# Kernel tuning notes

Hardware: AMD Instinct MI355X
Metric: run time of the kernel (lower is better)

Reference implementation:

```python
import jax, jax.numpy as jnp
import numpy as np

D_MODEL = 1024
N_HEADS = 16
D_K = D_MODEL // N_HEADS
D_FF = 4096
B = 2
T = 2048


def _layernorm(x, gamma, beta, eps=1e-5):
    mu = jnp.mean(x, axis=-1, keepdims=True)
    var = jnp.var(x, axis=-1, keepdims=True)
    return (x - mu) * jax.lax.rsqrt(var + eps) * gamma + beta


def _attention(q_in, kv_in, Wq, bq, Wk, bk, Wv, bv, mask):
    # q_in: [B,Tq,D], kv_in: [B,Tk,D]; Wq/Wk/Wv: [H,D,d_k]; b*: [H,d_k]
    Q = jnp.einsum('btd,hdk->bhtk', q_in, Wq) + bq[None, :, None, :]
    K = jnp.einsum('bsd,hdk->bhsk', kv_in, Wk) + bk[None, :, None, :]
    V = jnp.einsum('bsd,hdk->bhsk', kv_in, Wv) + bv[None, :, None, :]
    scores = jnp.einsum('bhtk,bhsk->bhts', Q, K) / jnp.sqrt(jnp.asarray(D_K, Q.dtype))
    if mask is not None:
        scores = jnp.where(mask, scores, jnp.finfo(scores.dtype).min)
    attn = jax.nn.softmax(scores, axis=-1)
    out = jnp.einsum('bhts,bhsk->bhtk', attn, V)  # [B,H,Tq,d_k]
    # concat heads: [B,Tq,H*d_k] == [B,Tq,D]
    return out.transpose(0, 2, 1, 3).reshape(q_in.shape[0], q_in.shape[1], -1)


def setup_inputs() -> dict:
    key = jax.random.key(0)
    ks = jax.random.split(key, 24)
    s = 0.02
    inp = {
        'dec_input': jax.random.normal(ks[0], (B, T, D_MODEL), jnp.float32),
        'enc_output': jax.random.normal(ks[1], (B, T, D_MODEL), jnp.float32),
        # self-attention per-head weights stacked over heads
        'Wq_s': jax.random.normal(ks[2], (N_HEADS, D_MODEL, D_K), jnp.float32) * s,
        'bq_s': jnp.zeros((N_HEADS, D_K), jnp.float32),
        'Wk_s': jax.random.normal(ks[3], (N_HEADS, D_MODEL, D_K), jnp.float32) * s,
        'bk_s': jnp.zeros((N_HEADS, D_K), jnp.float32),
        'Wv_s': jax.random.normal(ks[4], (N_HEADS, D_MODEL, D_K), jnp.float32) * s,
        'bv_s': jnp.zeros((N_HEADS, D_K), jnp.float32),
        'Wo_s': jax.random.normal(ks[5], (D_MODEL, D_MODEL), jnp.float32) * s,
        'bo_s': jnp.zeros((D_MODEL,), jnp.float32),
        # cross-attention per-head weights
        'Wq_c': jax.random.normal(ks[6], (N_HEADS, D_MODEL, D_K), jnp.float32) * s,
        'bq_c': jnp.zeros((N_HEADS, D_K), jnp.float32),
        'Wk_c': jax.random.normal(ks[7], (N_HEADS, D_MODEL, D_K), jnp.float32) * s,
        'bk_c': jnp.zeros((N_HEADS, D_K), jnp.float32),
        'Wv_c': jax.random.normal(ks[8], (N_HEADS, D_MODEL, D_K), jnp.float32) * s,
        'bv_c': jnp.zeros((N_HEADS, D_K), jnp.float32),
        'Wo_c': jax.random.normal(ks[9], (D_MODEL, D_MODEL), jnp.float32) * s,
        'bo_c': jnp.zeros((D_MODEL,), jnp.float32),
        # FFN
        'W1': jax.random.normal(ks[10], (D_MODEL, D_FF), jnp.float32) * s,
        'b1': jnp.zeros((D_FF,), jnp.float32),
        'W2': jax.random.normal(ks[11], (D_FF, D_MODEL), jnp.float32) * s,
        'b2': jnp.zeros((D_MODEL,), jnp.float32),
        # layernorms
        'g1': jnp.ones((D_MODEL,), jnp.float32), 'be1': jnp.zeros((D_MODEL,), jnp.float32),
        'g2': jnp.ones((D_MODEL,), jnp.float32), 'be2': jnp.zeros((D_MODEL,), jnp.float32),
        'g3': jnp.ones((D_MODEL,), jnp.float32), 'be3': jnp.zeros((D_MODEL,), jnp.float32),
    }
    return inp


def reference(dec_input, enc_output,
              Wq_s, bq_s, Wk_s, bk_s, Wv_s, bv_s, Wo_s, bo_s,
              Wq_c, bq_c, Wk_c, bk_c, Wv_c, bv_c, Wo_c, bo_c,
              W1, b1, W2, b2, g1, be1, g2, be2, g3, be3):
    Tq = dec_input.shape[1]
    causal = jnp.tril(jnp.ones((Tq, Tq), bool))[None, None, :, :]  # [1,1,T,T]
    # masked multi-head self-attention (dropout is identity in eval)
    sa = _attention(dec_input, dec_input, Wq_s, bq_s, Wk_s, bk_s, Wv_s, bv_s, causal)
    sa = sa @ Wo_s.T if False else jnp.einsum('btd,ed->bte', sa, Wo_s.T) if False else sa @ Wo_s + bo_s
    x1 = _layernorm(dec_input + sa, g1, be1)
    # cross-attention (no mask)
    ca = _attention(x1, enc_output, Wq_c, bq_c, Wk_c, bk_c, Wv_c, bv_c, None)
    ca = ca @ Wo_c + bo_c
    x2 = _layernorm(x1 + ca, g2, be2)
    # FFN
    ffn = jax.nn.relu(x2 @ W1 + b1) @ W2 + b2
    x3 = _layernorm(x2 + ffn, g3, be3)
    return x3
```

## Files before the change

### kernel.cpp

```cpp
#include <hip/hip_runtime.h>
#include <hip/hip_bf16.h>

typedef __attribute__((ext_vector_type(8))) short short8;
typedef __attribute__((ext_vector_type(4))) short short4v;
typedef __attribute__((ext_vector_type(4))) float floatx4;

#define TDIM 2048
#define BDIM 2
#define MROWS (BDIM * TDIM)

#define ASM_VMCNT0() __asm__ volatile("s_waitcnt vmcnt(0)" ::: "memory")
#define ASM_LGKM0()  __asm__ volatile("s_waitcnt lgkmcnt(0)" ::: "memory")
#define ASM_BARRIER() __asm__ volatile("s_barrier" ::: "memory")

__device__ __forceinline__ floatx4 mfma16(short4v a, short4v b, floatx4 c) {
#if defined(__HIP_DEVICE_COMPILE__)
#if __has_builtin(__builtin_amdgcn_mfma_f32_16x16x16bf16_1k)
    return __builtin_amdgcn_mfma_f32_16x16x16bf16_1k(a, b, c, 0, 0, 0);
#else
    short8 az = {a[0], a[1], a[2], a[3], 0, 0, 0, 0};
    short8 bz = {b[0], b[1], b[2], b[3], 0, 0, 0, 0};
    return __builtin_amdgcn_mfma_f32_16x16x32_bf16(az, bz, c, 0, 0, 0);
#endif
#else
    (void)a; (void)b;
    return c;
#endif
}

__device__ __forceinline__ void gload_lds16(const void* g, void* l) {
    __builtin_amdgcn_global_load_lds((const __attribute__((address_space(1))) void*)g,
                                     (__attribute__((address_space(3))) void*)l, 16, 0, 0);
}

__device__ __forceinline__ short bf16s(float x) {
    __hip_bfloat16 h = __float2bfloat16(x);
    return *(short*)&h;
}

__device__ __forceinline__ float fexp2(float x) {
#if defined(__HIP_DEVICE_COMPILE__)
#if __has_builtin(__builtin_amdgcn_exp2f)
    return __builtin_amdgcn_exp2f(x);
#else
    return exp2f(x);
#endif
#else
    return x;
#endif
}

__global__ __launch_bounds__(256) void cast2_k(const float* __restrict__ a,
                                               const float* __restrict__ b,
                                               __hip_bfloat16* __restrict__ oa,
                                               __hip_bfloat16* __restrict__ ob) {
    const int blk = blockIdx.x;
    const float* in = (blk < 4096) ? a : b;
    __hip_bfloat16* out = (blk < 4096) ? oa : ob;
    const size_t base = (size_t)(blk & 4095) * 1024 + threadIdx.x * 4;
    float4 v = *(const float4*)&in[base];
    out[base + 0] = __float2bfloat16(v.x);
    out[base + 1] = __float2bfloat16(v.y);
    out[base + 2] = __float2bfloat16(v.z);
    out[base + 3] = __float2bfloat16(v.w);
}

__device__ __forceinline__ void t32(float (*tile)[33], const float* __restrict__ in,
                                    __hip_bfloat16* __restrict__ out, int R, int C,
                                    int c0, int r0) {
    const int tx = threadIdx.x & 31, ty = threadIdx.x >> 5;
#pragma unroll
    for (int i = 0; i < 4; ++i)
        tile[ty + 8 * i][tx] = in[(size_t)(r0 + ty + 8 * i) * C + c0 + tx];
    __syncthreads();
#pragma unroll
    for (int i = 0; i < 4; ++i)
        out[(size_t)(c0 + ty + 8 * i) * R + r0 + tx] = __float2bfloat16(tile[tx][ty + 8 * i]);
}

__global__ __launch_bounds__(256) void prep_w_k(
    const float* __restrict__ Wq_s, const float* __restrict__ Wk_s, const float* __restrict__ Wv_s,
    const float* __restrict__ Wq_c, const float* __restrict__ Wk_c, const float* __restrict__ Wv_c,
    const float* __restrict__ Wo_s, const float* __restrict__ Wo_c,
    const float* __restrict__ W1, const float* __restrict__ W2,
    const float* __restrict__ bq_s, const float* __restrict__ bk_s, const float* __restrict__ bv_s,
    const float* __restrict__ bk_c, const float* __restrict__ bv_c,
    __hip_bfloat16* __restrict__ WtQKVs, __hip_bfloat16* __restrict__ WtQc,
    __hip_bfloat16* __restrict__ WtKVc, __hip_bfloat16* __restrict__ WtOs,
    __hip_bfloat16* __restrict__ WtOc, __hip_bfloat16* __restrict__ Wt1,
    __hip_bfloat16* __restrict__ Wt2,
    float* __restrict__ BiasQKVs, float* __restrict__ BiasKVc) {
    __shared__ float tile[32][33];
    const int t = blockIdx.x;
    if (t < 6144) {
        const int seg = t >> 10, tl = t & 1023;
        const float* s;
        __hip_bfloat16* d;
        if (seg == 0) { s = Wq_s; d = WtQKVs; }
        else if (seg == 1) { s = Wk_s; d = WtQKVs + 1048576; }
        else if (seg == 2) { s = Wv_s; d = WtQKVs + 2097152; }
        else if (seg == 3) { s = Wq_c; d = WtQc; }
        else if (seg == 4) { s = Wk_c; d = WtKVc; }
        else { s = Wv_c; d = WtKVc + 1048576; }
        const int slab = tl >> 6, rem = tl & 63;
        t32(tile, s + (size_t)slab * 65536, d + (size_t)slab * 65536, 1024, 64,
            (rem & 1) * 32, (rem >> 1) * 32);
    } else if (t < 8192) {
        const int rem = (t - 6144) & 1023;
        const float* s = (t < 7168) ? Wo_s : Wo_c;
        __hip_bfloat16* d = (t < 7168) ? WtOs : WtOc;
        t32(tile, s, d, 1024, 1024, (rem & 31) * 32, (rem >> 5) * 32);
    } else if (t < 12288) {
        const int rem = t - 8192;
        t32(tile, W1, Wt1, 1024, 4096, (rem & 127) * 32, (rem >> 7) * 32);
    } else if (t < 16384) {
        const int rem = t - 12288;
        t32(tile, W2, Wt2, 4096, 1024, (rem & 31) * 32, (rem >> 5) * 32);
    } else if (t < 16396) {
        const int i = (t - 16384) * 256 + threadIdx.x;
        BiasQKVs[i] = (i < 1024) ? bq_s[i] : (i < 2048 ? bk_s[i - 1024] : bv_s[i - 2048]);
    } else {
        const int i = (t - 16396) * 256 + threadIdx.x;
        BiasKVc[i] = (i < 1024) ? bk_c[i] : bv_c[i - 1024];
    }
}

__device__ __forceinline__ void gemm_core(
    const __hip_bfloat16* __restrict__ A, const __hip_bfloat16* __restrict__ Bt,
    int K, int kBeg, int kLen,
    const float* __restrict__ bias, __hip_bfloat16* __restrict__ C, int ldc,
    float* __restrict__ Pf,
    __hip_bfloat16* __restrict__ Vt, int vt_col0, int relu,
    int m0, int n0, __hip_bfloat16* sm) {
    const int tid = threadIdx.x;
    const int lane = tid & 63, wave = tid >> 6;
    const int quad = lane >> 4, l16 = lane & 15;
    const int wm = (wave >> 1) * 64, wn = (wave & 1) * 64;
    const int lrow = lane >> 3;
    const int gsw = (((lane & 7) ^ lrow)) * 8;
    const int sw7 = l16 & 7;
    const __hip_bfloat16* gA = A + (size_t)(m0 + wave * 32 + lrow) * K + kBeg + gsw;
    const __hip_bfloat16* gB = Bt + (size_t)(n0 + wave * 32 + lrow) * K + kBeg + gsw;
    __hip_bfloat16* lA = sm + wave * 2048;
    __hip_bfloat16* lB = sm + 16384 + wave * 2048;
    floatx4 acc[4][4] = {};
    const int T = kLen >> 6;
#pragma unroll
    for (int i = 0; i < 4; ++i) {
        gload_lds16(gA + (size_t)i * 8 * K, lA + i * 512);
        gload_lds16(gB + (size_t)i * 8 * K, lB + i * 512);
    }
    for (int t = 0; t < T; ++t) {
        ASM_VMCNT0();
        ASM_BARRIER();
        if (t + 1 < T) {
            const int koff = (t + 1) << 6;
            const int b = ((t + 1) & 1) * 8192;
#pragma unroll
            for (int i = 0; i < 4; ++i) {
                gload_lds16(gA + (size_t)i * 8 * K + koff, lA + b + i * 512);
                gload_lds16(gB + (size_t)i * 8 * K + koff, lB + b + i * 512);
            }
        }
        const __hip_bfloat16* cA = sm + (t & 1) * 8192;
        const __hip_bfloat16* cB = sm + 16384 + (t & 1) * 8192;
#pragma unroll
        for (int kc = 0; kc < 2; ++kc) {
            short8 af[4], bfr[4];
#pragma unroll
            for (int i = 0; i < 4; ++i) {
                af[i] = *(const short8*)&cA[(wm + i * 16 + l16) * 64 +
                                            (((kc * 4 + quad) ^ sw7) * 8)];
                bfr[i] = *(const short8*)&cB[(wn + i * 16 + l16) * 64 +
                                             (((kc * 4 + quad) ^ sw7) * 8)];
            }
#pragma unroll
            for (int mi = 0; mi < 4; ++mi)
#pragma unroll
                for (int ni = 0; ni < 4; ++ni)
                    acc[mi][ni] =
                        __builtin_amdgcn_mfma_f32_16x16x32_bf16(af[mi], bfr[ni], acc[mi][ni], 0, 0, 0);
        }
    }
    if (Pf) {
#pragma unroll
        for (int ni = 0; ni < 4; ++ni) {
            const int col = n0 + wn + ni * 16 + l16;
#pragma unroll
            for (int mi = 0; mi < 4; ++mi)
#pragma unroll
                for (int r = 0; r < 4; ++r) {
                    const int row = m0 + wm + mi * 16 + quad * 4 + r;
                    Pf[(size_t)row * ldc + col] = acc[mi][ni][r];
                }
        }
    } else {
        const bool toVt = (n0 >= vt_col0);
#pragma unroll
        for (int ni = 0; ni < 4; ++ni) {
            const int col = n0 + wn + ni * 16 + l16;
            const float bv = bias[col];
#pragma unroll
            for (int mi = 0; mi < 4; ++mi) {
                const int row0 = m0 + wm + mi * 16 + quad * 4;
                if (toVt) {
                    const int b = row0 >> 11, t0 = row0 & (TDIM - 1);
                    short4v pk;
#pragma unroll
                    for (int r = 0; r < 4; ++r) pk[r] = bf16s(acc[mi][ni][r] + bv);
                    *(short4v*)&Vt[((size_t)(b * 1024 + (col - vt_col0)) << 11) + t0] = pk;
                } else {
#pragma unroll
                    for (int r = 0; r < 4; ++r) {
                        float v = acc[mi][ni][r] + bv;
                        if (relu) v = fmaxf(v, 0.f);
                        C[(size_t)(row0 + r) * ldc + col] = __float2bfloat16(v);
                    }
                }
            }
        }
    }
}

__global__ __launch_bounds__(256) void gemm_bf16_k(const __hip_bfloat16* __restrict__ A,
                                                   const __hip_bfloat16* __restrict__ Bt,
                                                   const float* __restrict__ bias,
                                                   __hip_bfloat16* __restrict__ C,
                                                   int N, int K, int relu,
                                                   __hip_bfloat16* __restrict__ Vt, int vt_col0) {
    __shared__ __hip_bfloat16 sm[2 * 128 * 64 * 2];
    gemm_core(A, Bt, K, 0, K, bias, C, N, nullptr, Vt, vt_col0, relu,
              blockIdx.y * 128, blockIdx.x * 128, sm);
}

__global__ __launch_bounds__(256) void gemm_sk2_k(const __hip_bfloat16* __restrict__ A,
                                                  const __hip_bfloat16* __restrict__ Bt,
                                                  float* __restrict__ Pf, int N, int K) {
    __shared__ __hip_bfloat16 sm[2 * 128 * 64 * 2];
    const int z = blockIdx.z;
    gemm_core(A, Bt, K, z * (K >> 1), K >> 1, nullptr, nullptr, N,
              Pf + (size_t)z * MROWS * N, nullptr, 1 << 30, 0,
              blockIdx.y * 128, blockIdx.x * 128, sm);
}

__global__ __launch_bounds__(256) void gemm_pair_k(
    const __hip_bfloat16* __restrict__ A1, const __hip_bfloat16* __restrict__ Bt1,
    const float* __restrict__ bias1, __hip_bfloat16* __restrict__ C1, int N1, int K1,
    const __hip_bfloat16* __restrict__ A2, const __hip_bfloat16* __restrict__ Bt2,
    const float* __restrict__ bias2, __hip_bfloat16* __restrict__ C2, int N2, int K2,
    __hip_bfloat16* __restrict__ Vt2, int vtc2, int nx1) {
    __shared__ __hip_bfloat16 sm[2 * 128 * 64 * 2];
    if ((int)blockIdx.x < nx1)
        gemm_core(A1, Bt1, K1, 0, K1, bias1, C1, N1, nullptr, nullptr, 1 << 30, 0,
                  blockIdx.y * 128, blockIdx.x * 128, sm);
    else
        gemm_core(A2, Bt2, K2, 0, K2, bias2, C2, N2, nullptr, Vt2, vtc2, 0,
                  blockIdx.y * 128, (blockIdx.x - nx1) * 128, sm);
}

__device__ __forceinline__ void flash_one(
    const __hip_bfloat16* __restrict__ Q, int ldq, int qc0,
    const __hip_bfloat16* __restrict__ Kp, int ldk,
    const __hip_bfloat16* __restrict__ Vp,
    __hip_bfloat16* __restrict__ O, int causal, int q0, size_t rowb, int h,
    int tBeg, int tEnd, float* __restrict__ Opart, float* __restrict__ lpart,
    __hip_bfloat16* sK, __hip_bfloat16* sV) {
    const int tid = threadIdx.x, lane = tid & 63, wave = tid >> 6;
    const int quad = lane >> 4, l16 = lane & 15;
    const int lrow = lane >> 3;
    const int gsw = ((lane & 7) ^ lrow) * 8;
    const int sw7 = l16 & 7;
    short8 qf[2];
    {
        const __hip_bfloat16* qp = Q + (rowb + q0 + wave * 16 + l16) * (size_t)ldq + qc0 + h * 64;
        const float qs = 0.18033688f;
        short8 r0 = *(const short8*)(qp + quad * 8);
        short8 r1 = *(const short8*)(qp + 32 + quad * 8);
#pragma unroll
        for (int j = 0; j < 8; ++j) {
            qf[0][j] = bf16s(__uint_as_float(((unsigned)(unsigned short)r0[j]) << 16) * qs);
            qf[1][j] = bf16s(__uint_as_float(((unsigned)(unsigned short)r1[j]) << 16) * qs);
        }
    }
    short4v ones4;
#pragma unroll
    for (int j = 0; j < 4; ++j) ones4[j] = (short)0x3F80;
    floatx4 Ot[4] = {};
    floatx4 accl = {};
    const int nDiag = q0 >> 6;
    ASM_LGKM0();
    ASM_BARRIER();
    {
        const int s0 = tBeg << 6, pb = (tBeg & 1) * 4096;
#pragma unroll
        for (int i = 0; i < 2; ++i) {
            const int rb = wave * 16 + i * 8;
            gload_lds16(&Kp[(rowb + s0 + rb + lrow) * (size_t)ldk + gsw], &sK[pb + rb * 64]);
            gload_lds16(&Vp[(size_t)(rb + lrow) * TDIM + s0 + gsw], &sV[pb + rb * 64]);
        }
    }
    for (int t = tBeg; t < tEnd; ++t) {
        ASM_VMCNT0();
        ASM_BARRIER();
        if (t + 1 < tEnd) {
            const int s1 = (t + 1) << 6, nb = ((t + 1) & 1) * 4096;
#pragma unroll
            for (int i = 0; i < 2; ++i) {
                const int rb = wave * 16 + i * 8;
                gload_lds16(&Kp[(rowb + s1 + rb + lrow) * (size_t)ldk + gsw], &sK[nb + rb * 64]);
                gload_lds16(&Vp[(size_t)(rb + lrow) * TDIM + s1 + gsw], &sV[nb + rb * 64]);
            }
        }
        const int cb = (t & 1) * 4096;
        floatx4 Sf[4] = {};
#pragma unroll
        for (int st = 0; st < 4; ++st) {
            short8 b0 = *(const short8*)&sK[cb + (st * 16 + l16) * 64 + ((quad ^ sw7) * 8)];
            short8 b1 = *(const short8*)&sK[cb + (st * 16 + l16) * 64 + (((4 + quad) ^ sw7) * 8)];
            Sf[st] = __builtin_amdgcn_mfma_f32_16x16x32_bf16(b0, qf[0], Sf[st], 0, 0, 0);
            Sf[st] = __builtin_amdgcn_mfma_f32_16x16x32_bf16(b1, qf[1], Sf[st], 0, 0, 0);
        }
#pragma unroll
        for (int st = 0; st < 4; ++st)
#pragma unroll
            for (int r = 0; r < 4; ++r) Sf[st][r] = fexp2(Sf[st][r]);
        if (causal && t == nDiag) {
            const int qr = wave * 16 + l16;
#pragma unroll
            for (int st = 0; st < 4; ++st)
#pragma unroll
                for (int r = 0; r < 4; ++r)
                    if (st * 16 + quad * 4 + r > qr) Sf[st][r] = 0.f;
        }
        short4v pf[4];
#pragma unroll
        for (int st = 0; st < 4; ++st)
#pragma unroll
            for (int r = 0; r < 4; ++r) pf[st][r] = bf16s(Sf[st][r]);
#pragma unroll
        for (int st = 0; st < 4; ++st) accl = mfma16(ones4, pf[st], accl);
#pragma unroll
        for (int dt = 0; dt < 4; ++dt)
#pragma unroll
            for (int st = 0; st < 4; ++st) {
                short4v av = *(const short4v*)&sV[cb + (dt * 16 + l16) * 64 +
                                                 (((st * 2 + (quad >> 1)) ^ sw7) * 8) +
                                                 (quad & 1) * 4];
                Ot[dt] = mfma16(av, pf[st], Ot[dt]);
            }
    }
    if (Opart) {
        const int qrow = wave * 16 + l16;
#pragma unroll
        for (int dt = 0; dt < 4; ++dt)
            *(floatx4*)&Opart[qrow * 64 + dt * 16 + quad * 4] = Ot[dt];
        if (quad == 0) lpart[qrow] = accl[0];
    } else {
        const float inv = 1.0f / accl[0];
        __hip_bfloat16* op = O + (rowb + q0 + wave * 16 + l16) * (size_t)1024 + h * 64 + quad * 4;
#pragma unroll
        for (int dt = 0; dt < 4; ++dt) {
            short4v pk;
#pragma unroll
            for (int r = 0; r < 4; ++r) pk[r] = bf16s(Ot[dt][r] * inv);
            *(short4v*)(op + dt * 16) = pk;
        }
    }
}

__global__ __launch_bounds__(256) void flash_attn(const __hip_bfloat16* __restrict__ Q, int ldq, int qc0,
                                                  const __hip_bfloat16* __restrict__ K, int ldk, int kc0,
                                                  const __hip_bfloat16* __restrict__ Vt,
                                                  __hip_bfloat16* __restrict__ O, int causal,
                                                  float* __restrict__ Opart,
                                                  float* __restrict__ lpart) {
    __shared__ __hip_bfloat16 sK[2 * 64 * 64];
    __shared__ __hip_bfloat16 sV[2 * 64 * 64];
    const int bh = blockIdx.y, b = bh >> 4, h = bh & 15;
    const size_t rowb = (size_t)b * TDIM;
    const __hip_bfloat16* Kp = K + kc0 + h * 64;
    const __hip_bfloat16* Vp = Vt + ((size_t)(b * 1024 + h * 64) << 11);
    if (causal) {
        const int bx = blockIdx.x;
        if (bx < 32) {
            const int i = 16 + (bx >> 1), hh = bx & 1;
            const int n = i + 1, n2 = n >> 1;
            const int p = bh * 16 + (i - 16);
            float* Op = Opart + (size_t)p * 8192 + hh * 4096;
            float* lp = lpart + p * 128 + hh * 64;
            flash_one(Q, ldq, qc0, Kp, ldk, Vp, O, 1, i * 64, rowb, h,
                      hh ? n2 : 0, hh ? n : n2, Op, lp, sK, sV);
        } else {
            const int i = 47 - bx;
            flash_one(Q, ldq, qc0, Kp, ldk, Vp, O, 1, i * 64, rowb, h,
                      0, i + 1, nullptr, nullptr, sK, sV);
        }
    } else {
        flash_one(Q, ldq, qc0, Kp, ldk, Vp, O, 0, (int)blockIdx.x * 64, rowb, h,
                  0, TDIM >> 6, nullptr, nullptr, sK, sV);
    }
}

__global__ __launch_bounds__(256) void fa_combine_k(const float* __restrict__ Opart,
                                                    const float* __restrict__ lpart,
                                                    __hip_bfloat16* __restrict__ O) {
    const int p = blockIdx.x;
    const int bh = p >> 4, i = (p & 15) + 16;
    const int b = bh >> 4, h = bh & 15;
    const int tid = threadIdx.x;
    const int q = tid >> 2, dseg = (tid & 3) * 16;
    const float* O0 = Opart + (size_t)p * 8192;
    const float* O1 = O0 + 4096;
    const float inv = 1.f / (lpart[p * 128 + q] + lpart[p * 128 + 64 + q]);
    __hip_bfloat16* op = O + ((size_t)(b * TDIM) + i * 64 + q) * 1024 + h * 64 + dseg;
#pragma unroll
    for (int j = 0; j < 4; ++j) {
        floatx4 a = *(const floatx4*)&O0[q * 64 + dseg + j * 4];
        floatx4 c = *(const floatx4*)&O1[q * 64 + dseg + j * 4];
        short4v pk;
#pragma unroll
        for (int r = 0; r < 4; ++r) pk[r] = bf16s((a[r] + c[r]) * inv);
        *(short4v*)(op + j * 4) = pk;
    }
}

__global__ __launch_bounds__(256) void ln2_k(const float* __restrict__ resid,
                                             const float* __restrict__ d0,
                                             const float* __restrict__ d1,
                                             const float* __restrict__ biasN,
                                             const float* __restrict__ gamma,
                                             const float* __restrict__ beta,
                                             float* __restrict__ outf,
                                             __hip_bfloat16* __restrict__ outb) {
    const int row = blockIdx.x, tid = threadIdx.x;
    const size_t base = (size_t)row * 1024;
    float x[4], s = 0.f, sq = 0.f;
#pragma unroll
    for (int i = 0; i < 4; ++i) {
        const int c = tid + 256 * i;
        x[i] = resid[base + c] + d0[base + c] + d1[base + c] + biasN[c];
        s += x[i];
        sq += x[i] * x[i];
    }
#pragma unroll
    for (int off = 32; off > 0; off >>= 1) {
        s += __shfl_down(s, off);
        sq += __shfl_down(sq, off);
    }
    __shared__ float red[8];
    if ((tid & 63) == 0) {
        red[tid >> 6] = s;
        red[4 + (tid >> 6)] = sq;
    }
    __syncthreads();
    const float S = red[0] + red[1] + red[2] + red[3];
    const float Q2 = red[4] + red[5] + red[6] + red[7];
    const float mean = S * (1.f / 1024.f);
    const float var = Q2 * (1.f / 1024.f) - mean * mean;
    const float rstd = rsqrtf(var + 1e-5f);
#pragma unroll
    for (int i = 0; i < 4; ++i) {
        const int c = tid + 256 * i;
        const float y = (x[i] - mean) * rstd * gamma[c] + beta[c];
        outf[base + c] = y;
        if (outb) outb[base + c] = __float2bfloat16(y);
    }
}

extern "C" void kernel_launch(void* const* d_in, const int* in_sizes, int n_in,
                              void* d_out, int out_size, void* d_ws, size_t ws_size,
                              hipStream_t stream) {
    (void)in_sizes; (void)n_in; (void)out_size; (void)ws_size;
    const float* dec  = (const float*)d_in[0];
    const float* enc  = (const float*)d_in[1];
    const float* Wq_s = (const float*)d_in[2];
    const float* bq_s = (const float*)d_in[3];
    const float* Wk_s = (const float*)d_in[4];
    const float* bk_s = (const float*)d_in[5];
    const float* Wv_s = (const float*)d_in[6];
    const float* bv_s = (const float*)d_in[7];
    const float* Wo_s = (const float*)d_in[8];
    const float* bo_s = (const float*)d_in[9];
    const float* Wq_c = (const float*)d_in[10];
    const float* bq_c = (const float*)d_in[11];
    const float* Wk_c = (const float*)d_in[12];
    const float* bk_c = (const float*)d_in[13];
    const float* Wv_c = (const float*)d_in[14];
    const float* bv_c = (const float*)d_in[15];
    const float* Wo_c = (const float*)d_in[16];
    const float* bo_c = (const float*)d_in[17];
    const float* W1   = (const float*)d_in[18];
    const float* b1   = (const float*)d_in[19];
    const float* W2   = (const float*)d_in[20];
    const float* b2   = (const float*)d_in[21];
    const float* g1   = (const float*)d_in[22];
    const float* be1  = (const float*)d_in[23];
    const float* g2   = (const float*)d_in[24];
    const float* be2  = (const float*)d_in[25];
    const float* g3   = (const float*)d_in[26];
    const float* be3  = (const float*)d_in[27];

    char* w = (char*)d_ws;
    const size_t MB = 1ull << 20;
    __hip_bfloat16* Xdec   = (__hip_bfloat16*)(w + 0 * MB);
    __hip_bfloat16* Xenc   = (__hip_bfloat16*)(w + 8 * MB);
    __hip_bfloat16* WtQKVs = (__hip_bfloat16*)(w + 16 * MB);
    __hip_bfloat16* WtOs   = (__hip_bfloat16*)(w + 22 * MB);
    __hip_bfloat16* WtQc   = (__hip_bfloat16*)(w + 24 * MB);
    __hip_bfloat16* WtKVc  = (__hip_bfloat16*)(w + 26 * MB);
    __hip_bfloat16* WtOc   = (__hip_bfloat16*)(w + 30 * MB);
    __hip_bfloat16* Wt1    = (__hip_bfloat16*)(w + 32 * MB);
    __hip_bfloat16* Wt2    = (__hip_bfloat16*)(w + 40 * MB);
    float*          BiasQKVs = (float*)(w + 48 * MB);
    float*          BiasKVc  = (float*)(w + 48 * MB + 65536);
    __hip_bfloat16* QKV    = (__hip_bfloat16*)(w + 49 * MB);
    __hip_bfloat16* Qc     = QKV;
    __hip_bfloat16* KVc    = (__hip_bfloat16*)(w + 57 * MB);
    float*          Psplit = (float*)(w + 49 * MB);
    __hip_bfloat16* VtBuf  = (__hip_bfloat16*)(w + 73 * MB);
    __hip_bfloat16* Attn   = (__hip_bfloat16*)(w + 81 * MB);
    float*          X1f    = (float*)(w + 97 * MB);
    __hip_bfloat16* X1b    = (__hip_bfloat16*)(w + 113 * MB);
    float*          X2f    = (float*)(w + 121 * MB);
    __hip_bfloat16* X2b    = (__hip_bfloat16*)(w + 137 * MB);
    __hip_bfloat16* H1     = (__hip_bfloat16*)(w + 145 * MB);
    float*          FaO    = (float*)(w + 145 * MB);
    float*          FaL    = (float*)(w + 161 * MB);
    float*          P0     = Psplit;
    float*          P1     = Psplit + (size_t)MROWS * 1024;
    const int NOVT = 1 << 30;

    cast2_k<<<8192, 256, 0, stream>>>(dec, enc, Xdec, Xenc);
    prep_w_k<<<16404, 256, 0, stream>>>(Wq_s, Wk_s, Wv_s, Wq_c, Wk_c, Wv_c, Wo_s, Wo_c,
                                        W1, W2, bq_s, bk_s, bv_s, bk_c, bv_c,
                                        WtQKVs, WtQc, WtKVc, WtOs, WtOc, Wt1, Wt2,
                                        BiasQKVs, BiasKVc);

    gemm_bf16_k<<<dim3(24, 32), 256, 0, stream>>>(Xdec, WtQKVs, BiasQKVs, QKV, 3072, 1024, 0,
                                                  VtBuf, 2048);
    flash_attn<<<dim3(48, 32), 256, 0, stream>>>(QKV, 3072, 0, QKV, 3072, 1024, VtBuf, Attn, 1,
                                                 FaO, FaL);
    fa_combine_k<<<512, 256, 0, stream>>>(FaO, FaL, Attn);
    gemm_sk2_k<<<dim3(8, 32, 2), 256, 0, stream>>>(Attn, WtOs, Psplit, 1024, 1024);
    ln2_k<<<MROWS, 256, 0, stream>>>(dec, P0, P1, bo_s, g1, be1, X1f, X1b);

    gemm_pair_k<<<dim3(24, 32), 256, 0, stream>>>(X1b, WtQc, bq_c, Qc, 1024, 1024,
                                                  Xenc, WtKVc, BiasKVc, KVc, 2048, 1024,
                                                  VtBuf, 1024, 8);
    flash_attn<<<dim3(32, 32), 256, 0, stream>>>(Qc, 1024, 0, KVc, 2048, 0, VtBuf, Attn, 0,
                                                 nullptr, nullptr);
    gemm_sk2_k<<<dim3(8, 32, 2), 256, 0, stream>>>(Attn, WtOc, Psplit, 1024, 1024);
    ln2_k<<<MROWS, 256, 0, stream>>>(X1f, P0, P1, bo_c, g2, be2, X2f, X2b);

    gemm_bf16_k<<<dim3(32, 32), 256, 0, stream>>>(X2b, Wt1, b1, H1, 4096, 1024, 1,
                                                  (__hip_bfloat16*)nullptr, NOVT);
    gemm_sk2_k<<<dim3(8, 32, 2), 256, 0, stream>>>(H1, Wt2, Psplit, 1024, 4096);
    ln2_k<<<MROWS, 256, 0, stream>>>(X2f, P0, P1, b2, g3, be3, (float*)d_out, (__hip_bfloat16*)nullptr);
}
```

Before: 527.1 us.

## Use 256x256-tile 8-wave GEMM kernel for QKV, cross-attn projections and FFN

```diff
diff --git a/kernel.cpp b/kernel.cpp
--- a/kernel.cpp
+++ b/kernel.cpp
@@ -10,6 +10,7 @@
 #define MROWS (BDIM * TDIM)
 
 #define ASM_VMCNT0() __asm__ volatile("s_waitcnt vmcnt(0)" ::: "memory")
+#define ASM_VMCNT2() __asm__ volatile("s_waitcnt vmcnt(2)" ::: "memory")
 #define ASM_LGKM0()  __asm__ volatile("s_waitcnt lgkmcnt(0)" ::: "memory")
 #define ASM_BARRIER() __asm__ volatile("s_barrier" ::: "memory")
 
@@ -222,17 +223,6 @@
     }
 }
 
-__global__ __launch_bounds__(256) void gemm_bf16_k(const __hip_bfloat16* __restrict__ A,
-                                                   const __hip_bfloat16* __restrict__ Bt,
-                                                   const float* __restrict__ bias,
-                                                   __hip_bfloat16* __restrict__ C,
-                                                   int N, int K, int relu,
-                                                   __hip_bfloat16* __restrict__ Vt, int vt_col0) {
-    __shared__ __hip_bfloat16 sm[2 * 128 * 64 * 2];
-    gemm_core(A, Bt, K, 0, K, bias, C, N, nullptr, Vt, vt_col0, relu,
-              blockIdx.y * 128, blockIdx.x * 128, sm);
-}
-
 __global__ __launch_bounds__(256) void gemm_sk2_k(const __hip_bfloat16* __restrict__ A,
                                                   const __hip_bfloat16* __restrict__ Bt,
                                                   float* __restrict__ Pf, int N, int K) {
@@ -243,19 +233,170 @@
               blockIdx.y * 128, blockIdx.x * 128, sm);
 }
 
-__global__ __launch_bounds__(256) void gemm_pair_k(
+__device__ __forceinline__ void gemm256_core(
+    const __hip_bfloat16* __restrict__ A, const __hip_bfloat16* __restrict__ Bt,
+    int K, int kBeg, int kLen,
+    const float* __restrict__ bias, __hip_bfloat16* __restrict__ C, int ldc,
+    float* __restrict__ Pf,
+    __hip_bfloat16* __restrict__ Vt, int vt_col0, int relu,
+    int m0, int n0, __hip_bfloat16* sm) {
+    const int tid = threadIdx.x;
+    const int lane = tid & 63, wave = tid >> 6;
+    const int quad = lane >> 4, l16 = lane & 15;
+    const int wm = (wave >> 2) * 128, wn = (wave & 3) * 64;
+    const int lrow = lane >> 3;
+    const int gsw = ((lane & 7) ^ lrow) * 8;
+    const int sw7 = l16 & 7;
+    const __hip_bfloat16* aSrc = A + (size_t)(m0 + wave * 16 + lrow) * K + kBeg + gsw;
+    const __hip_bfloat16* bSrc = Bt + (size_t)(n0 + wave * 16 + lrow) * K + kBeg + gsw;
+    floatx4 acc[8][4] = {};
+    const int T = kLen >> 6;
+#pragma unroll
+    for (int h = 0; h < 2; ++h)
+#pragma unroll
+        for (int j = 0; j < 2; ++j) {
+            const size_t ro = (size_t)(h * 128 + j * 8);
+            gload_lds16(aSrc + ro * K, sm + (h * 128 + wave * 16 + j * 8) * 64);
+            gload_lds16(bSrc + ro * K, sm + 16384 + (h * 128 + wave * 16 + j * 8) * 64);
+        }
+    for (int t = 0; t < T; ++t) {
+        const int c = t & 1;
+        const int nt = (t + 1 < T) ? (t + 1) : t;
+        const size_t nko = (size_t)nt * 64;
+        __hip_bfloat16* dst = sm + (1 - c) * 32768;
+        const __hip_bfloat16* cA = sm + c * 32768;
+        const __hip_bfloat16* cB = cA + 16384;
+        ASM_BARRIER();
+#pragma unroll
+        for (int j = 0; j < 2; ++j)
+            gload_lds16(aSrc + (size_t)(j * 8) * K + nko, dst + (wave * 16 + j * 8) * 64);
+        ASM_VMCNT2();
+        ASM_BARRIER();
+        short8 af[4], bfr[4];
+#pragma unroll
+        for (int i = 0; i < 4; ++i) {
+            af[i] = *(const short8*)&cA[(wm + i * 16 + l16) * 64 + ((quad ^ sw7) * 8)];
+            bfr[i] = *(const short8*)&cB[(wn + i * 16 + l16) * 64 + ((quad ^ sw7) * 8)];
+        }
+        __builtin_amdgcn_s_setprio(1);
+#pragma unroll
+        for (int mi = 0; mi < 4; ++mi)
+#pragma unroll
+            for (int ni = 0; ni < 4; ++ni)
+                acc[mi][ni] = __builtin_amdgcn_mfma_f32_16x16x32_bf16(af[mi], bfr[ni], acc[mi][ni], 0, 0, 0);
+        __builtin_amdgcn_s_setprio(0);
+        ASM_BARRIER();
+#pragma unroll
+        for (int i = 0; i < 4; ++i)
+            af[i] = *(const short8*)&cA[(wm + 64 + i * 16 + l16) * 64 + ((quad ^ sw7) * 8)];
+#pragma unroll
+        for (int j = 0; j < 2; ++j)
+            gload_lds16(aSrc + (size_t)(128 + j * 8) * K + nko, dst + (128 + wave * 16 + j * 8) * 64);
+        __builtin_amdgcn_s_setprio(1);
+#pragma unroll
+        for (int mi = 0; mi < 4; ++mi)
+#pragma unroll
+            for (int ni = 0; ni < 4; ++ni)
+                acc[4 + mi][ni] = __builtin_amdgcn_mfma_f32_16x16x32_bf16(af[mi], bfr[ni], acc[4 + mi][ni], 0, 0, 0);
+        __builtin_amdgcn_s_setprio(0);
+        ASM_BARRIER();
+#pragma unroll
+        for (int i = 0; i < 4; ++i) {
+            af[i] = *(const short8*)&cA[(wm + i * 16 + l16) * 64 + (((4 + quad) ^ sw7) * 8)];
+            bfr[i] = *(const short8*)&cB[(wn + i * 16 + l16) * 64 + (((4 + quad) ^ sw7) * 8)];
+        }
+#pragma unroll
+        for (int j = 0; j < 2; ++j)
+            gload_lds16(bSrc + (size_t)(j * 8) * K + nko, dst + 16384 + (wave * 16 + j * 8) * 64);
+        __builtin_amdgcn_s_setprio(1);
+#pragma unroll
+        for (int mi = 0; mi < 4; ++mi)
+#pragma unroll
+            for (int ni = 0; ni < 4; ++ni)
+                acc[mi][ni] = __builtin_amdgcn_mfma_f32_16x16x32_bf16(af[mi], bfr[ni], acc[mi][ni], 0, 0, 0);
+        __builtin_amdgcn_s_setprio(0);
+        ASM_BARRIER();
+#pragma unroll
+        for (int i = 0; i < 4; ++i)
+            af[i] = *(const short8*)&cA[(wm + 64 + i * 16 + l16) * 64 + (((4 + quad) ^ sw7) * 8)];
+#pragma unroll
+        for (int j = 0; j < 2; ++j)
+            gload_lds16(bSrc + (size_t)(128 + j * 8) * K + nko, dst + 16384 + (128 + wave * 16 + j * 8) * 64);
+        __builtin_amdgcn_s_setprio(1);
+#pragma unroll
+        for (int mi = 0; mi < 4; ++mi)
+#pragma unroll
+            for (int ni = 0; ni < 4; ++ni)
+                acc[4 + mi][ni] = __builtin_amdgcn_mfma_f32_16x16x32_bf16(af[mi], bfr[ni], acc[4 + mi][ni], 0, 0, 0);
+        __builtin_amdgcn_s_setprio(0);
+    }
+    if (Pf) {
+#pragma unroll
+        for (int ni = 0; ni < 4; ++ni) {
+            const int col = n0 + wn + ni * 16 + l16;
+#pragma unroll
+            for (int mi = 0; mi < 8; ++mi)
+#pragma unroll
+                for (int r = 0; r < 4; ++r) {
+                    const int row = m0 + wm + mi * 16 + quad * 4 + r;
+                    Pf[(size_t)row * ldc + col] = acc[mi][ni][r];
+                }
+        }
+    } else {
+        const bool toVt = (n0 >= vt_col0);
+#pragma unroll
+        for (int ni = 0; ni < 4; ++ni) {
+            const int col = n0 + wn + ni * 16 + l16;
+            const float bv = bias[col];
+#pragma unroll
+            for (int mi = 0; mi < 8; ++mi) {
+                const int row0 = m0 + wm + mi * 16 + quad * 4;
+                if (toVt) {
+                    const int b = row0 >> 11, t0 = row0 & (TDIM - 1);
+                    short4v pk;
+#pragma unroll
+                    for (int r = 0; r < 4; ++r) pk[r] = bf16s(acc[mi][ni][r] + bv);
+                    *(short4v*)&Vt[((size_t)(b * 1024 + (col - vt_col0)) << 11) + t0] = pk;
+                } else {
+#pragma unroll
+                    for (int r = 0; r < 4; ++r) {
+                        float v = acc[mi][ni][r] + bv;
+                        if (relu) v = fmaxf(v, 0.f);
+                        C[(size_t)(row0 + r) * ldc + col] = __float2bfloat16(v);
+                    }
+                }
+            }
+        }
+    }
+}
+
+__global__ __launch_bounds__(512, 2) void g256_k(const __hip_bfloat16* __restrict__ A,
+                                                 const __hip_bfloat16* __restrict__ Bt,
+                                                 const float* __restrict__ bias,
+                                                 __hip_bfloat16* __restrict__ C,
+                                                 int N, int K, int kSplit, int relu,
+                                                 __hip_bfloat16* __restrict__ Vt, int vt_col0,
+                                                 float* __restrict__ Pf) {
+    __shared__ __hip_bfloat16 sm[65536];
+    const int z = blockIdx.z;
+    float* pf = Pf ? Pf + (size_t)z * MROWS * N : nullptr;
+    gemm256_core(A, Bt, K, z * kSplit, kSplit, bias, C, N, pf, Vt, vt_col0, relu,
+                 blockIdx.y * 256, blockIdx.x * 256, sm);
+}
+
+__global__ __launch_bounds__(512, 2) void g256_pair_k(
     const __hip_bfloat16* __restrict__ A1, const __hip_bfloat16* __restrict__ Bt1,
     const float* __restrict__ bias1, __hip_bfloat16* __restrict__ C1, int N1, int K1,
     const __hip_bfloat16* __restrict__ A2, const __hip_bfloat16* __restrict__ Bt2,
     const float* __restrict__ bias2, __hip_bfloat16* __restrict__ C2, int N2, int K2,
     __hip_bfloat16* __restrict__ Vt2, int vtc2, int nx1) {
-    __shared__ __hip_bfloat16 sm[2 * 128 * 64 * 2];
+    __shared__ __hip_bfloat16 sm[65536];
     if ((int)blockIdx.x < nx1)
-        gemm_core(A1, Bt1, K1, 0, K1, bias1, C1, N1, nullptr, nullptr, 1 << 30, 0,
-                  blockIdx.y * 128, blockIdx.x * 128, sm);
+        gemm256_core(A1, Bt1, K1, 0, K1, bias1, C1, N1, nullptr, nullptr, 1 << 30, 0,
+                     blockIdx.y * 256, blockIdx.x * 256, sm);
     else
-        gemm_core(A2, Bt2, K2, 0, K2, bias2, C2, N2, nullptr, Vt2, vtc2, 0,
-                  blockIdx.y * 128, (blockIdx.x - nx1) * 128, sm);
+        gemm256_core(A2, Bt2, K2, 0, K2, bias2, C2, N2, nullptr, Vt2, vtc2, 0,
+                     blockIdx.y * 256, (blockIdx.x - nx1) * 256, sm);
 }
 
 __device__ __forceinline__ void flash_one(
@@ -536,24 +677,25 @@
                                         WtQKVs, WtQc, WtKVc, WtOs, WtOc, Wt1, Wt2,
                                         BiasQKVs, BiasKVc);
 
-    gemm_bf16_k<<<dim3(24, 32), 256, 0, stream>>>(Xdec, WtQKVs, BiasQKVs, QKV, 3072, 1024, 0,
-                                                  VtBuf, 2048);
+    g256_k<<<dim3(12, 16, 1), 512, 0, stream>>>(Xdec, WtQKVs, BiasQKVs, QKV, 3072, 1024, 1024, 0,
+                                                VtBuf, 2048, nullptr);
     flash_attn<<<dim3(48, 32), 256, 0, stream>>>(QKV, 3072, 0, QKV, 3072, 1024, VtBuf, Attn, 1,
                                                  FaO, FaL);
     fa_combine_k<<<512, 256, 0, stream>>>(FaO, FaL, Attn);
     gemm_sk2_k<<<dim3(8, 32, 2), 256, 0, stream>>>(Attn, WtOs, Psplit, 1024, 1024);
     ln2_k<<<MROWS, 256, 0, stream>>>(dec, P0, P1, bo_s, g1, be1, X1f, X1b);
 
-    gemm_pair_k<<<dim3(24, 32), 256, 0, stream>>>(X1b, WtQc, bq_c, Qc, 1024, 1024,
-                                                  Xenc, WtKVc, BiasKVc, KVc, 2048, 1024,
-                                                  VtBuf, 1024, 8);
+    g256_pair_k<<<dim3(12, 16, 1), 512, 0, stream>>>(X1b, WtQc, bq_c, Qc, 1024, 1024,
+                                                     Xenc, WtKVc, BiasKVc, KVc, 2048, 1024,
+                                                     VtBuf, 1024, 4);
     flash_attn<<<dim3(32, 32), 256, 0, stream>>>(Qc, 1024, 0, KVc, 2048, 0, VtBuf, Attn, 0,
                                                  nullptr, nullptr);
     gemm_sk2_k<<<dim3(8, 32, 2), 256, 0, stream>>>(Attn, WtOc, Psplit, 1024, 1024);
     ln2_k<<<MROWS, 256, 0, stream>>>(X1f, P0, P1, bo_c, g2, be2, X2f, X2b);
 
-    gemm_bf16_k<<<dim3(32, 32), 256, 0, stream>>>(X2b, Wt1, b1, H1, 4096, 1024, 1,
-                                                  (__hip_bfloat16*)nullptr, NOVT);
-    gemm_sk2_k<<<dim3(8, 32, 2), 256, 0, stream>>>(H1, Wt2, Psplit, 1024, 4096);
+    g256_k<<<dim3(16, 16, 1), 512, 0, stream>>>(X2b, Wt1, b1, H1, 4096, 1024, 1024, 1,
+                                                nullptr, NOVT, nullptr);
+    g256_k<<<dim3(4, 16, 2), 512, 0, stream>>>(H1, Wt2, nullptr, nullptr, 1024, 4096, 2048, 0,
+                                               nullptr, NOVT, Psplit);
     ln2_k<<<MROWS, 256, 0, stream>>>(X2f, P0, P1, b2, g3, be3, (float*)d_out, (__hip_bfloat16*)nullptr);
 }
```

Result: no change. 533.2 us (+1.2%).
